# Kernel optimization log

Hardware: AMD Instinct MI355X
Metric: run time of the kernel (lower is better)

## Reference

```python
import jax, jax.numpy as jnp
import numpy as np

EPS = 1e-3  # keras LayerNormalization default epsilon


def layer_norm(x, g, b):
    mu = jnp.mean(x, axis=-1, keepdims=True)
    var = jnp.mean(jnp.square(x - mu), axis=-1, keepdims=True)
    return g * (x - mu) / jnp.sqrt(var + EPS) + b


def setup_inputs() -> dict:
    key = jax.random.key(0)
    ks = jax.random.split(key, 16)
    B, S, E, H, F = 2, 4096, 512, 8, 2048
    s_e = 1.0 / np.sqrt(E)
    s_f = 1.0 / np.sqrt(F)
    inp = {
        "x": jax.random.normal(ks[0], (B, S, E), dtype=jnp.float32),
        "WQ": jax.random.normal(ks[1], (E, E), dtype=jnp.float32) * s_e,
        "bQ": jnp.zeros((E,), jnp.float32),
        "WK": jax.random.normal(ks[2], (E, E), dtype=jnp.float32) * s_e,
        "bK": jnp.zeros((E,), jnp.float32),
        "WV": jax.random.normal(ks[3], (E, E), dtype=jnp.float32) * s_e,
        "bV": jnp.zeros((E,), jnp.float32),
        "WO": jax.random.normal(ks[4], (E, E), dtype=jnp.float32) * s_e,
        "bO": jnp.zeros((E,), jnp.float32),
        "W1": jax.random.normal(ks[5], (E, F), dtype=jnp.float32) * s_e,
        "b1": jnp.zeros((F,), jnp.float32),
        "W2": jax.random.normal(ks[6], (F, E), dtype=jnp.float32) * s_f,
        "b2": jnp.zeros((E,), jnp.float32),
        "g1": jnp.ones((E,), jnp.float32),
        "beta1": jnp.zeros((E,), jnp.float32),
        "g2": jnp.ones((E,), jnp.float32),
        "beta2": jnp.zeros((E,), jnp.float32),
        "num_head": 8,
    }
    return inp


def reference(x, WQ, bQ, WK, bK, WV, bV, WO, bO, W1, b1, W2, b2,
              g1, beta1, g2, beta2, num_head):
    B, S, E = x.shape
    H = num_head
    d = E // H
    scale = jnp.sqrt(jnp.asarray(d, jnp.float32))

    q = (x @ WQ + bQ).reshape(B, S, H, d).transpose(0, 2, 1, 3)  # [B,H,S,d]
    k = (x @ WK + bK).reshape(B, S, H, d).transpose(0, 2, 1, 3)
    v = (x @ WV + bV).reshape(B, S, H, d).transpose(0, 2, 1, 3)

    score = jnp.einsum('bhqd,bhkd->bhqk', q, k) / scale  # O(S^2) materialized, as in source
    attn = jax.nn.softmax(score, axis=-1)
    zs = jnp.einsum('bhqk,bhkd->bhqd', attn, v)  # [B,H,S,d]

    # Faithful to source bug: reshape [B,H,S,d] -> [B,S,E] WITHOUT transposing back
    zs = zs.reshape(B, S, E)
    zs = zs @ WO + bO

    z = layer_norm(zs + x, g1, beta1)
    r = jax.nn.relu(z @ W1 + b1) @ W2 + b2
    r = layer_norm(r + z, g2, beta2)
    return r
```

## Files before the change

### kernel.cpp

```cpp
#include <hip/hip_runtime.h>
#include <hip/hip_bf16.h>

typedef unsigned short u16;
typedef __attribute__((ext_vector_type(8))) short bf16x8;
typedef __attribute__((ext_vector_type(4))) float f32x4;
typedef __attribute__((ext_vector_type(16))) float f32x16;

static constexpr int BB = 2;
static constexpr int SS = 4096;
static constexpr int EE = 512;
static constexpr int HH = 8;
static constexpr int DD = 64;
static constexpr int FF = 2048;
static constexpr int NR = BB * SS;
static constexpr int QS = 3 * EE;

#define QSCALE 0.18033688011112042f

__device__ __forceinline__ u16 f2bf(float f) {
  union { float f; unsigned u; } v; v.f = f;
  unsigned r = v.u + 0x7FFFu + ((v.u >> 16) & 1u);
  return (u16)(r >> 16);
}
__device__ __forceinline__ unsigned pack2(float a, float b) {
  return (unsigned)f2bf(a) | ((unsigned)f2bf(b) << 16);
}
__device__ __forceinline__ unsigned cvtpk(float lo, float hi) {
  unsigned r;
  asm("v_cvt_pk_bf16_f32 %0, %1, %2" : "=v"(r) : "v"(lo), "v"(hi));
  return r;
}
__device__ __forceinline__ void perm32swap(unsigned& a, unsigned& b) {
  asm("v_permlane32_swap_b32 %0, %1" : "+v"(a), "+v"(b));
}
__device__ __forceinline__ void gload_lds16(const u16* g, u16* l) {
  __builtin_amdgcn_global_load_lds(
      (const __attribute__((address_space(1))) unsigned*)g,
      (__attribute__((address_space(3))) unsigned*)l, 16, 0, 0);
}

struct TrJob { const float* W; u16* Wt; int K, N, k0, n0; };

__device__ __forceinline__ void transp_tile(const float* W, u16* Wt, int K,
                                            int N, int k0, int n0, int t) {
  __shared__ float T[64][65];
  const int tn = t & 63, tk = t >> 6;
#pragma unroll
  for (int i = 0; i < 16; ++i) {
    int kk = tk * 16 + i;
    T[kk][tn] = W[(size_t)(k0 + kk) * N + n0 + tn];
  }
  __syncthreads();
#pragma unroll
  for (int i = 0; i < 16; ++i) {
    int nn = tk * 16 + i;
    Wt[(size_t)(n0 + nn) * K + k0 + tn] = f2bf(T[tn][nn]);
  }
}

__global__ __launch_bounds__(256) void prep_all(
    const float* __restrict__ x, u16* __restrict__ xb,
    const float* __restrict__ WQ, const float* __restrict__ WK,
    const float* __restrict__ WV, const float* __restrict__ WO,
    const float* __restrict__ W1, const float* __restrict__ W2,
    u16* __restrict__ Wqkv_t, u16* __restrict__ WO_t, u16* __restrict__ W1_t,
    u16* __restrict__ W2_t, const float* __restrict__ bQ,
    const float* __restrict__ bK, const float* __restrict__ bV,
    float* __restrict__ bqkv) {
  const int bx = blockIdx.x;
  const int t = threadIdx.x;
  if (bx < 2048) {
    int i = (bx * 256 + t) * 8;
    float4 a = *(const float4*)(x + i);
    float4 b = *(const float4*)(x + i + 4);
    uint4 u;
    u.x = pack2(a.x, a.y); u.y = pack2(a.z, a.w);
    u.z = pack2(b.x, b.y); u.w = pack2(b.z, b.w);
    *(uint4*)(xb + i) = u;
    return;
  }
  int idx = bx - 2048;
  if (idx < 768) {
    TrJob j;
    if (idx < 256) {
      const float* srcs[4] = {WQ, WK, WV, WO};
      u16* dsts[4] = {Wqkv_t, Wqkv_t + 512 * 512, Wqkv_t + 1024 * 512, WO_t};
      int w = idx >> 6, l = idx & 63;
      j = {srcs[w], dsts[w], 512, 512, (l & 7) * 64, (l >> 3) * 64};
    } else if (idx < 512) {
      int l = idx - 256;
      j = {W1, W1_t, 512, 2048, (l & 7) * 64, (l >> 3) * 64};
    } else {
      int l = idx - 512;
      j = {W2, W2_t, 2048, 512, (l & 31) * 64, (l >> 5) * 64};
    }
    transp_tile(j.W, j.Wt, j.K, j.N, j.k0, j.n0, t);
    return;
  }
  for (int i = t; i < QS; i += 256)
    bqkv[i] = i < 512 ? bQ[i] : (i < 1024 ? bK[i - 512] : bV[i - 1024]);
}

__global__ __launch_bounds__(256) void transp_v(const u16* __restrict__ qkvb,
                                                u16* __restrict__ vt) {
  __shared__ u16 T[64][72];
  const int s0 = blockIdx.x * 64, c0 = blockIdx.y * 64, b = blockIdx.z;
  const int t = threadIdx.x;
#pragma unroll
  for (int i = 0; i < 2; ++i) {
    int idx = t + i * 256;
    int row = idx >> 3, c8 = idx & 7;
    *(uint4*)(&T[row][c8 * 8]) = *(const uint4*)(
        &qkvb[((size_t)b * SS + s0 + row) * QS + 1024 + c0 + c8 * 8]);
  }
  __syncthreads();
#pragma unroll
  for (int i = 0; i < 2; ++i) {
    int idx = t + i * 256;
    int c = idx >> 3, s8 = idx & 7;
    u16 tmp[8];
#pragma unroll
    for (int j = 0; j < 8; ++j) tmp[j] = T[s8 * 8 + j][c];
    *(uint4*)(&vt[((size_t)b * EE + c0 + c) * SS + s0 + s8 * 8]) =
        *(uint4*)tmp;
  }
}

template <int RELU, int OUT_BF16, int SCALEQ = 0>
__global__ __launch_bounds__(256) void gemm64(
    const u16* __restrict__ A, const u16* __restrict__ Bt,
    const float* __restrict__ bias, void* __restrict__ Cout,
    int M, int N, int K) {
  __shared__ __align__(16) u16 As[2][64 * 64];
  __shared__ __align__(16) u16 Bs[2][64 * 64];
  const int t = threadIdx.x;
  const int lane = t & 63, wid = t >> 6;
  const int lm = lane & 15, lg = lane >> 4;
  const int bm = blockIdx.x * 64, bn = blockIdx.y * 64;
  const int wr = (wid >> 1) * 32, wc = (wid & 1) * 32;
  const int sr = lane >> 3;
  const int scb = (lane & 7) ^ sr;

  f32x4 acc[2][2];
#pragma unroll
  for (int i = 0; i < 2; ++i)
#pragma unroll
    for (int j = 0; j < 2; ++j) acc[i][j] = (f32x4){0.f, 0.f, 0.f, 0.f};

  auto stage = [&](int kb, int buf) {
#pragma unroll
    for (int i = 0; i < 2; ++i) {
      int r8 = wid * 16 + i * 8;
      gload_lds16(A + (size_t)(bm + r8 + sr) * K + kb + scb * 8,
                  &As[buf][r8 * 64]);
      gload_lds16(Bt + (size_t)(bn + r8 + sr) * K + kb + scb * 8,
                  &Bs[buf][r8 * 64]);
    }
  };

  stage(0, 0);
  const int nsteps = K >> 6;
  for (int s = 0; s < nsteps; ++s) {
    const int cur = s & 1;
    __syncthreads();
    if (s + 1 < nsteps) stage((s + 1) << 6, cur ^ 1);

#pragma unroll
    for (int c = 0; c < 2; ++c) {
      bf16x8 af[2], bfr[2];
#pragma unroll
      for (int i = 0; i < 2; ++i) {
        int ar = wr + i * 16 + lm;
        af[i] = *(const bf16x8*)(
            &As[cur][ar * 64 + (((c * 4 + lg) ^ (ar & 7)) << 3)]);
        int br = wc + i * 16 + lm;
        bfr[i] = *(const bf16x8*)(
            &Bs[cur][br * 64 + (((c * 4 + lg) ^ (br & 7)) << 3)]);
      }
#pragma unroll
      for (int i = 0; i < 2; ++i)
#pragma unroll
        for (int j = 0; j < 2; ++j)
          acc[i][j] = __builtin_amdgcn_mfma_f32_16x16x32_bf16(
              af[i], bfr[j], acc[i][j], 0, 0, 0);
    }
  }

  float bi[2];
#pragma unroll
  for (int j = 0; j < 2; ++j) bi[j] = bias[bn + wc + j * 16 + lm];

#pragma unroll
  for (int i = 0; i < 2; ++i) {
#pragma unroll
    for (int j = 0; j < 2; ++j) {
      int col = bn + wc + j * 16 + lm;
#pragma unroll
      for (int r = 0; r < 4; ++r) {
        int row = bm + wr + i * 16 + lg * 4 + r;
        float vv = acc[i][j][r] + bi[j];
        if (RELU) vv = fmaxf(vv, 0.f);
        if (SCALEQ && col < 512) vv *= QSCALE;
        if (OUT_BF16)
          ((u16*)Cout)[(size_t)row * N + col] = f2bf(vv);
        else
          ((float*)Cout)[(size_t)row * N + col] = vv;
      }
    }
  }
}

__global__ __launch_bounds__(128) void attn_mfma(
    const u16* __restrict__ qkv, const u16* __restrict__ vt,
    u16* __restrict__ zs) {
  __shared__ __align__(16) u16 K_lds[2][64 * 64];
  __shared__ __align__(16) u16 V_lds[2][64 * 64];
  __shared__ float Linv[2][32];

  const int qblock = blockIdx.x;
  const int bh = blockIdx.y;
  const int b = bh >> 3, h = bh & 7;
  const int t = threadIdx.x;
  const int lane = t & 63, wid = t >> 6;
  const int q32 = lane & 31, hi = lane >> 5;
  const int qs7 = q32 & 7;
  const size_t bS = (size_t)b * SS;
  const u16* kp = qkv + 512;
  const u16* vrow = vt + ((size_t)b * EE + h * DD) * SS;
  const int qbase = qblock * 64 + wid * 32;

  bf16x8 qf[4];
  {
    const u16* qrow = qkv + (bS + qbase + q32) * QS + h * DD + hi * 8;
#pragma unroll
    for (int c = 0; c < 4; ++c) qf[c] = *(const bf16x8*)(qrow + c * 16);
  }

  const int sr = lane >> 3;
  const int scb = (lane & 7) ^ sr;

  f32x16 o0, o1;
#pragma unroll
  for (int i = 0; i < 16; ++i) { o0[i] = 0.f; o1[i] = 0.f; }
  float lsum = 0.f;

  auto stage = [&](int kt, int bufi) {
#pragma unroll
    for (int i = 0; i < 4; ++i) {
      int rbase = wid * 32 + i * 8;
      gload_lds16(kp + (bS + kt * 64 + rbase + sr) * QS + h * DD + scb * 8,
                  &K_lds[bufi][rbase * 64]);
      gload_lds16(vrow + (size_t)(rbase + sr) * SS + kt * 64 + scb * 8,
                  &V_lds[bufi][rbase * 64]);
    }
  };

  stage(0, 0);

  for (int kt = 0; kt < SS / 64; ++kt) {
    const int cur = kt & 1;
    __syncthreads();
    if (kt + 1 < SS / 64) stage(kt + 1, cur ^ 1);

    float p[2][16];
#pragma unroll
    for (int blk = 0; blk < 2; ++blk) {
      f32x16 s;
#pragma unroll
      for (int i = 0; i < 16; ++i) s[i] = 0.f;
      const int krow = blk * 32 + q32;
      __builtin_amdgcn_s_setprio(1);
#pragma unroll
      for (int c = 0; c < 4; ++c) {
        bf16x8 kf = *(const bf16x8*)(
            &K_lds[cur][krow * 64 + (((2 * c + hi) ^ qs7) << 3)]);
        s = __builtin_amdgcn_mfma_f32_32x32x16_bf16(kf, qf[c], s, 0, 0, 0);
      }
      __builtin_amdgcn_s_setprio(0);
#pragma unroll
      for (int r = 0; r < 16; ++r) {
        p[blk][r] = __builtin_amdgcn_exp2f(s[r]);
        lsum += p[blk][r];
      }
    }

    __builtin_amdgcn_s_setprio(1);
#pragma unroll
    for (int kc = 0; kc < 4; ++kc) {
      const int bb = kc >> 1, rA = (kc & 1) * 8, rB = rA + 4;
      unsigned wA0 = cvtpk(p[bb][rA + 0], p[bb][rA + 1]);
      unsigned wA1 = cvtpk(p[bb][rA + 2], p[bb][rA + 3]);
      unsigned wB0 = cvtpk(p[bb][rB + 0], p[bb][rB + 1]);
      unsigned wB1 = cvtpk(p[bb][rB + 2], p[bb][rB + 3]);
      perm32swap(wA0, wB0);
      perm32swap(wA1, wB1);
      union { unsigned u[4]; bf16x8 v; } pf;
      pf.u[0] = wA0; pf.u[1] = wA1; pf.u[2] = wB0; pf.u[3] = wB1;
      bf16x8 vf0 = *(const bf16x8*)(
          &V_lds[cur][q32 * 64 + (((2 * kc + hi) ^ qs7) << 3)]);
      bf16x8 vf1 = *(const bf16x8*)(
          &V_lds[cur][(32 + q32) * 64 + (((2 * kc + hi) ^ qs7) << 3)]);
      o0 = __builtin_amdgcn_mfma_f32_32x32x16_bf16(pf.v, vf0, o0, 0, 0, 0);
      o1 = __builtin_amdgcn_mfma_f32_32x32x16_bf16(pf.v, vf1, o1, 0, 0, 0);
    }
    __builtin_amdgcn_s_setprio(0);
  }

  float fl = lsum + __shfl_xor(lsum, 32);
  if (lane < 32) Linv[wid][q32] = 1.f / fl;

#pragma unroll
  for (int reg = 0; reg < 16; ++reg) {
    int q = (reg & 3) + 8 * (reg >> 2) + 4 * hi;
    float inv = Linv[wid][q];
    int s = qbase + q;
    u16* dst = zs + ((size_t)b * SS + h * 512 + (s >> 3)) * EE + (s & 7) * 64;
    dst[q32] = f2bf(o0[reg] * inv);
    dst[32 + q32] = f2bf(o1[reg] * inv);
  }
}

template <int WB>
__global__ __launch_bounds__(128) void add_ln(
    const float* __restrict__ a, const float* __restrict__ xres,
    const float* __restrict__ g, const float* __restrict__ beta,
    float* __restrict__ outf, u16* __restrict__ outb) {
  const int row = blockIdx.x;
  const int tid = threadIdx.x;
  const float4 av = *(const float4*)(a + (size_t)row * EE + tid * 4);
  const float4 xv = *(const float4*)(xres + (size_t)row * EE + tid * 4);
  float vx = av.x + xv.x, vy = av.y + xv.y, vz = av.z + xv.z, vw = av.w + xv.w;
  float sum = vx + vy + vz + vw;
  float sq = vx * vx + vy * vy + vz * vz + vw * vw;
#pragma unroll
  for (int off = 1; off < 64; off <<= 1) {
    sum += __shfl_xor(sum, off);
    sq += __shfl_xor(sq, off);
  }
  __shared__ float s0[2], s1[2];
  int w = tid >> 6;
  if ((tid & 63) == 0) { s0[w] = sum; s1[w] = sq; }
  __syncthreads();
  sum = s0[0] + s0[1];
  sq = s1[0] + s1[1];
  float mu = sum * (1.0f / EE);
  float var = sq * (1.0f / EE) - mu * mu;
  float r = rsqrtf(var + 1e-3f);
  int c = tid * 4;
  float4 gv = *(const float4*)(g + c);
  float4 bv = *(const float4*)(beta + c);
  float4 ov;
  ov.x = gv.x * (vx - mu) * r + bv.x;
  ov.y = gv.y * (vy - mu) * r + bv.y;
  ov.z = gv.z * (vz - mu) * r + bv.z;
  ov.w = gv.w * (vw - mu) * r + bv.w;
  *(float4*)(outf + (size_t)row * EE + c) = ov;
  if (WB) {
    uint2 u;
    u.x = pack2(ov.x, ov.y);
    u.y = pack2(ov.z, ov.w);
    *(uint2*)(outb + (size_t)row * EE + c) = u;
  }
}

extern "C" void kernel_launch(void* const* d_in, const int* in_sizes, int n_in,
                              void* d_out, int out_size, void* d_ws,
                              size_t ws_size, hipStream_t stream) {
  const float* x = (const float*)d_in[0];
  const float* WQ = (const float*)d_in[1];
  const float* bQ = (const float*)d_in[2];
  const float* WK = (const float*)d_in[3];
  const float* bK = (const float*)d_in[4];
  const float* WV = (const float*)d_in[5];
  const float* bV = (const float*)d_in[6];
  const float* WO = (const float*)d_in[7];
  const float* bO = (const float*)d_in[8];
  const float* W1 = (const float*)d_in[9];
  const float* b1 = (const float*)d_in[10];
  const float* W2 = (const float*)d_in[11];
  const float* b2 = (const float*)d_in[12];
  const float* g1 = (const float*)d_in[13];
  const float* be1 = (const float*)d_in[14];
  const float* g2 = (const float*)d_in[15];
  const float* be2 = (const float*)d_in[16];
  float* out = (float*)d_out;

  const size_t MB = 1u << 20;
  char* w = (char*)d_ws;
  u16* Wqkv_t = (u16*)(w + 0);
  u16* WO_t   = (u16*)(w + 2 * MB);
  u16* W1_t   = (u16*)(w + 3 * MB);
  u16* W2_t   = (u16*)(w + 5 * MB);
  float* bqkv = (float*)(w + 7 * MB);
  u16* qkvb = (u16*)(w + 8 * MB);
  u16* zsb  = (u16*)(w + 32 * MB);
  float* zs2 = (float*)(w + 40 * MB);
  float* z   = (float*)(w + 56 * MB);
  u16* zb    = (u16*)(w + 72 * MB);
  u16* xb    = (u16*)(w + 80 * MB);
  u16* vtb   = (u16*)(w + 88 * MB);
  u16* f1    = (u16*)(w + 8 * MB);
  float* f2  = zs2;

  dim3 blk(256);

  prep_all<<<dim3(2817), blk, 0, stream>>>(x, xb, WQ, WK, WV, WO, W1, W2,
                                           Wqkv_t, WO_t, W1_t, W2_t, bQ, bK,
                                           bV, bqkv);

  gemm64<0, 1, 1><<<dim3(128, 24), blk, 0, stream>>>(xb, Wqkv_t, bqkv, qkvb,
                                                     NR, QS, EE);
  transp_v<<<dim3(SS / 64, EE / 64, BB), blk, 0, stream>>>(qkvb, vtb);
  attn_mfma<<<dim3(SS / 64, BB * HH), dim3(128), 0, stream>>>(qkvb, vtb, zsb);
  gemm64<0, 0><<<dim3(128, 8), blk, 0, stream>>>(zsb, WO_t, bO, zs2,
                                                 NR, EE, EE);
  add_ln<1><<<dim3(NR), dim3(128), 0, stream>>>(zs2, x, g1, be1, z, zb);
  gemm64<1, 1><<<dim3(128, 32), blk, 0, stream>>>(zb, W1_t, b1, f1,
                                                  NR, FF, EE);
  gemm64<0, 0><<<dim3(128, 8), blk, 0, stream>>>(f1, W2_t, b2, f2,
                                                 NR, EE, FF);
  add_ln<0><<<dim3(NR), dim3(128), 0, stream>>>(f2, z, g2, be2, out, nullptr);
}
```

Measured before the change: 231.2 us.

## Use bf16 intermediates for residual/LayerNorm path and interleave attention softmax with PV

The WO and W2 GEMMs now write bf16 instead of fp32, and the LayerNorm kernels read bf16 inputs and residuals (the bf16 copy of x and z) instead of fp32, which halves the memory traffic of those stages. Separately, the attention loop now uses incremental K/V pointers and interleaves the second QK MFMA block with the exp and PV of the first block to overlap transcendental work with matrix ops. The cost is extra rounding error in the residual and LayerNorm inputs, which may move the output away from the fp32 reference.

```diff
diff --git a/kernel.cpp b/kernel.cpp
--- a/kernel.cpp
+++ b/kernel.cpp
@@ -24,6 +24,12 @@
 }
 __device__ __forceinline__ unsigned pack2(float a, float b) {
   return (unsigned)f2bf(a) | ((unsigned)f2bf(b) << 16);
+}
+__device__ __forceinline__ float bf2f_lo(unsigned u) {
+  union { unsigned u; float f; } v; v.u = u << 16; return v.f;
+}
+__device__ __forceinline__ float bf2f_hi(unsigned u) {
+  union { unsigned u; float f; } v; v.u = u & 0xffff0000u; return v.f;
 }
 __device__ __forceinline__ unsigned cvtpk(float lo, float hi) {
   unsigned r;
@@ -225,8 +231,6 @@
   const int q32 = lane & 31, hi = lane >> 5;
   const int qs7 = q32 & 7;
   const size_t bS = (size_t)b * SS;
-  const u16* kp = qkv + 512;
-  const u16* vrow = vt + ((size_t)b * EE + h * DD) * SS;
   const int qbase = qblock * 64 + wid * 32;
 
   bf16x8 qf[4];
@@ -239,32 +243,42 @@
   const int sr = lane >> 3;
   const int scb = (lane & 7) ^ sr;
 
+  const u16* kcur = qkv + 512 + bS * QS + h * DD;
+  const u16* vcur = vt + ((size_t)b * EE + h * DD) * SS;
+  size_t koff[4], voff[4];
+#pragma unroll
+  for (int i = 0; i < 4; ++i) {
+    int rbase = wid * 32 + i * 8 + sr;
+    koff[i] = (size_t)rbase * QS + scb * 8;
+    voff[i] = (size_t)rbase * SS + scb * 8;
+  }
+
   f32x16 o0, o1;
 #pragma unroll
   for (int i = 0; i < 16; ++i) { o0[i] = 0.f; o1[i] = 0.f; }
   float lsum = 0.f;
 
-  auto stage = [&](int kt, int bufi) {
+  auto stage = [&](int bufi) {
 #pragma unroll
     for (int i = 0; i < 4; ++i) {
       int rbase = wid * 32 + i * 8;
-      gload_lds16(kp + (bS + kt * 64 + rbase + sr) * QS + h * DD + scb * 8,
-                  &K_lds[bufi][rbase * 64]);
-      gload_lds16(vrow + (size_t)(rbase + sr) * SS + kt * 64 + scb * 8,
-                  &V_lds[bufi][rbase * 64]);
+      gload_lds16(kcur + koff[i], &K_lds[bufi][rbase * 64]);
+      gload_lds16(vcur + voff[i], &V_lds[bufi][rbase * 64]);
     }
   };
 
-  stage(0, 0);
+  stage(0);
 
   for (int kt = 0; kt < SS / 64; ++kt) {
     const int cur = kt & 1;
     __syncthreads();
-    if (kt + 1 < SS / 64) stage(kt + 1, cur ^ 1);
-
-    float p[2][16];
-#pragma unroll
-    for (int blk = 0; blk < 2; ++blk) {
+    if (kt + 1 < SS / 64) {
+      kcur += 64 * QS;
+      vcur += 64;
+      stage(cur ^ 1);
+    }
+
+    auto qk = [&](int blk) -> f32x16 {
       f32x16 s;
 #pragma unroll
       for (int i = 0; i < 16; ++i) s[i] = 0.f;
@@ -277,21 +291,14 @@
         s = __builtin_amdgcn_mfma_f32_32x32x16_bf16(kf, qf[c], s, 0, 0, 0);
       }
       __builtin_amdgcn_s_setprio(0);
-#pragma unroll
-      for (int r = 0; r < 16; ++r) {
-        p[blk][r] = __builtin_amdgcn_exp2f(s[r]);
-        lsum += p[blk][r];
-      }
-    }
-
-    __builtin_amdgcn_s_setprio(1);
-#pragma unroll
-    for (int kc = 0; kc < 4; ++kc) {
-      const int bb = kc >> 1, rA = (kc & 1) * 8, rB = rA + 4;
-      unsigned wA0 = cvtpk(p[bb][rA + 0], p[bb][rA + 1]);
-      unsigned wA1 = cvtpk(p[bb][rA + 2], p[bb][rA + 3]);
-      unsigned wB0 = cvtpk(p[bb][rB + 0], p[bb][rB + 1]);
-      unsigned wB1 = cvtpk(p[bb][rB + 2], p[bb][rB + 3]);
+      return s;
+    };
+    auto pv = [&](const float* p, int kc) {
+      const int rA = (kc & 1) * 8, rB = rA + 4;
+      unsigned wA0 = cvtpk(p[rA + 0], p[rA + 1]);
+      unsigned wA1 = cvtpk(p[rA + 2], p[rA + 3]);
+      unsigned wB0 = cvtpk(p[rB + 0], p[rB + 1]);
+      unsigned wB1 = cvtpk(p[rB + 2], p[rB + 3]);
       perm32swap(wA0, wB0);
       perm32swap(wA1, wB1);
       union { unsigned u[4]; bf16x8 v; } pf;
@@ -300,10 +307,30 @@
           &V_lds[cur][q32 * 64 + (((2 * kc + hi) ^ qs7) << 3)]);
       bf16x8 vf1 = *(const bf16x8*)(
           &V_lds[cur][(32 + q32) * 64 + (((2 * kc + hi) ^ qs7) << 3)]);
+      __builtin_amdgcn_s_setprio(1);
       o0 = __builtin_amdgcn_mfma_f32_32x32x16_bf16(pf.v, vf0, o0, 0, 0, 0);
       o1 = __builtin_amdgcn_mfma_f32_32x32x16_bf16(pf.v, vf1, o1, 0, 0, 0);
-    }
-    __builtin_amdgcn_s_setprio(0);
+      __builtin_amdgcn_s_setprio(0);
+    };
+
+    f32x16 s0 = qk(0);
+    float p0[16];
+#pragma unroll
+    for (int r = 0; r < 16; ++r) {
+      p0[r] = __builtin_amdgcn_exp2f(s0[r]);
+      lsum += p0[r];
+    }
+    f32x16 s1 = qk(1);
+    pv(p0, 0);
+    pv(p0, 1);
+    float p1[16];
+#pragma unroll
+    for (int r = 0; r < 16; ++r) {
+      p1[r] = __builtin_amdgcn_exp2f(s1[r]);
+      lsum += p1[r];
+    }
+    pv(p1, 2);
+    pv(p1, 3);
   }
 
   float fl = lsum + __shfl_xor(lsum, 32);
@@ -320,16 +347,19 @@
   }
 }
 
-template <int WB>
-__global__ __launch_bounds__(128) void add_ln(
-    const float* __restrict__ a, const float* __restrict__ xres,
+template <int WF32>
+__global__ __launch_bounds__(128) void add_ln_b(
+    const u16* __restrict__ a, const u16* __restrict__ xres,
     const float* __restrict__ g, const float* __restrict__ beta,
-    float* __restrict__ outf, u16* __restrict__ outb) {
+    u16* __restrict__ outb, float* __restrict__ outf) {
   const int row = blockIdx.x;
   const int tid = threadIdx.x;
-  const float4 av = *(const float4*)(a + (size_t)row * EE + tid * 4);
-  const float4 xv = *(const float4*)(xres + (size_t)row * EE + tid * 4);
-  float vx = av.x + xv.x, vy = av.y + xv.y, vz = av.z + xv.z, vw = av.w + xv.w;
+  uint2 av = *(const uint2*)(a + (size_t)row * EE + tid * 4);
+  uint2 xv = *(const uint2*)(xres + (size_t)row * EE + tid * 4);
+  float vx = bf2f_lo(av.x) + bf2f_lo(xv.x);
+  float vy = bf2f_hi(av.x) + bf2f_hi(xv.x);
+  float vz = bf2f_lo(av.y) + bf2f_lo(xv.y);
+  float vw = bf2f_hi(av.y) + bf2f_hi(xv.y);
   float sum = vx + vy + vz + vw;
   float sq = vx * vx + vy * vy + vz * vz + vw * vw;
 #pragma unroll
@@ -349,16 +379,17 @@
   int c = tid * 4;
   float4 gv = *(const float4*)(g + c);
   float4 bv = *(const float4*)(beta + c);
-  float4 ov;
-  ov.x = gv.x * (vx - mu) * r + bv.x;
-  ov.y = gv.y * (vy - mu) * r + bv.y;
-  ov.z = gv.z * (vz - mu) * r + bv.z;
-  ov.w = gv.w * (vw - mu) * r + bv.w;
-  *(float4*)(outf + (size_t)row * EE + c) = ov;
-  if (WB) {
+  float o0 = gv.x * (vx - mu) * r + bv.x;
+  float o1 = gv.y * (vy - mu) * r + bv.y;
+  float o2 = gv.z * (vz - mu) * r + bv.z;
+  float o3 = gv.w * (vw - mu) * r + bv.w;
+  if (WF32) {
+    float4 ov = {o0, o1, o2, o3};
+    *(float4*)(outf + (size_t)row * EE + c) = ov;
+  } else {
     uint2 u;
-    u.x = pack2(ov.x, ov.y);
-    u.y = pack2(ov.z, ov.w);
+    u.x = pack2(o0, o1);
+    u.y = pack2(o2, o3);
     *(uint2*)(outb + (size_t)row * EE + c) = u;
   }
 }
@@ -394,13 +425,12 @@
   float* bqkv = (float*)(w + 7 * MB);
   u16* qkvb = (u16*)(w + 8 * MB);
   u16* zsb  = (u16*)(w + 32 * MB);
-  float* zs2 = (float*)(w + 40 * MB);
-  float* z   = (float*)(w + 56 * MB);
-  u16* zb    = (u16*)(w + 72 * MB);
-  u16* xb    = (u16*)(w + 80 * MB);
-  u16* vtb   = (u16*)(w + 88 * MB);
-  u16* f1    = (u16*)(w + 8 * MB);
-  float* f2  = zs2;
+  u16* zs2b = (u16*)(w + 40 * MB);
+  u16* f2b  = (u16*)(w + 48 * MB);
+  u16* zb   = (u16*)(w + 72 * MB);
+  u16* xb   = (u16*)(w + 80 * MB);
+  u16* vtb  = (u16*)(w + 88 * MB);
+  u16* f1   = (u16*)(w + 8 * MB);
 
   dim3 blk(256);
 
@@ -412,12 +442,14 @@
                                                      NR, QS, EE);
   transp_v<<<dim3(SS / 64, EE / 64, BB), blk, 0, stream>>>(qkvb, vtb);
   attn_mfma<<<dim3(SS / 64, BB * HH), dim3(128), 0, stream>>>(qkvb, vtb, zsb);
-  gemm64<0, 0><<<dim3(128, 8), blk, 0, stream>>>(zsb, WO_t, bO, zs2,
+  gemm64<0, 1><<<dim3(128, 8), blk, 0, stream>>>(zsb, WO_t, bO, zs2b,
                                                  NR, EE, EE);
-  add_ln<1><<<dim3(NR), dim3(128), 0, stream>>>(zs2, x, g1, be1, z, zb);
+  add_ln_b<0><<<dim3(NR), dim3(128), 0, stream>>>(zs2b, xb, g1, be1, zb,
+                                                  nullptr);
   gemm64<1, 1><<<dim3(128, 32), blk, 0, stream>>>(zb, W1_t, b1, f1,
                                                   NR, FF, EE);
-  gemm64<0, 0><<<dim3(128, 8), blk, 0, stream>>>(f1, W2_t, b2, f2,
+  gemm64<0, 1><<<dim3(128, 8), blk, 0, stream>>>(f1, W2_t, b2, f2b,
                                                  NR, EE, FF);
-  add_ln<0><<<dim3(NR), dim3(128), 0, stream>>>(f2, z, g2, be2, out, nullptr);
-}
+  add_ln_b<1><<<dim3(NR), dim3(128), 0, stream>>>(f2b, zb, g2, be2, nullptr,
+                                                  out);
+}
```

Measured after the change: 228.2 us. No clear change (-1.3%).
